# Optimization experiments

Measured on AMD Instinct MI355X. Metric: run time of the kernel, lower is better.

## Reference

```python
import jax, jax.numpy as jnp
import numpy as np

NEG_SLOPE = 0.2
CLAMP = 1e9

C, N, T, IN_F = 8, 1024, 3, 64
H, OUT_F = 4, 64
E = 65536


def setup_inputs() -> dict:
    key = jax.random.key(0)
    k1, k2, k3, k4, k5 = jax.random.split(key, 5)
    edge_idx = jax.random.randint(k1, (2, E), 0, C * N, dtype=jnp.int64)
    node_feats = jax.random.normal(k2, (C, N, T, IN_F), dtype=jnp.float32)
    # xavier-ish scaling for parameters
    fc = jax.random.normal(k3, (T, IN_F, OUT_F * H), dtype=jnp.float32) * (2.0 / (IN_F + OUT_F * H)) ** 0.5
    attn_src = jax.random.normal(k4, (1, H, OUT_F * T), dtype=jnp.float32) * 0.1
    attn_dst = jax.random.normal(k5, (1, H, OUT_F * T), dtype=jnp.float32) * 0.1
    return {"edge_idx": edge_idx, "node_feats": node_feats, "fc": fc,
            "attn_src": attn_src, "attn_dst": attn_dst}


def reference(edge_idx, node_feats, fc, attn_src, attn_dst):
    c, n, t, f_in = node_feats.shape
    h = attn_src.shape[1]
    f_out = fc.shape[2] // h
    cn = c * n

    # per-node-type linear transform: (cn, t, in) x (t, in, h*out) -> (cn, t, h*out)
    hs = node_feats.reshape(cn, t, f_in)
    feat = jnp.einsum('bji,jik->bjk', hs, fc)

    # replicate the torch permute/reshape sequence exactly (row-major reshapes)
    x = feat.reshape(c, n, t, f_out * h)
    x = jnp.transpose(x, (0, 2, 1, 3))                  # (c, t, n, h*out)
    x = x.reshape(c, n, t, h, f_out)                    # torch .reshape on permuted copy
    x = jnp.transpose(x, (0, 1, 3, 2, 4))               # (c, n, h, t, out)
    feat_flat = x.reshape(cn, h, t * f_out)             # feat_src = feat_dst

    # node masks from edge endpoints (scatter 1s on rows)
    msrc = jnp.zeros((cn,), node_feats.dtype).at[edge_idx[0]].set(1.0)
    mdst = jnp.zeros((cn,), node_feats.dtype).at[edge_idx[1]].set(1.0)
    feat_src = feat_flat * msrc[:, None, None]
    feat_dst = feat_flat * mdst[:, None, None]

    a_src = jnp.clip(feat_src * attn_src, -CLAMP, CLAMP).reshape(c, n, h, f_out * t).sum(-1)
    a_dst = jnp.clip(feat_dst * attn_dst, -CLAMP, CLAMP).reshape(c, n, h, f_out * t).sum(-1)

    a = a_src[:, :, None, :] + a_dst[:, None, :, :]     # (c, n, n, h)
    a = jnp.where(a >= 0, a, NEG_SLOPE * a)             # leaky relu
    a = jnp.clip(a, -CLAMP, CLAMP)
    a = jax.nn.softmax(a, axis=0)                       # softmax over conformers (dim=0, as in source)

    fd = feat_dst.reshape(c, n, h, t * f_out)
    m = jnp.einsum('cvuh,cuhf->cvhf', a, fd)            # (c, n, h, t*out)
    m = jax.nn.relu(m)
    outs = m.reshape(c, n, h, t, f_out).sum(axis=2)     # (c, n, t, out)
    return outs, a
```

## Files before the change

### kernel.cpp

```cpp
#include <hip/hip_runtime.h>
#include <stdint.h>

#define CC 8
#define NN 1024
#define CN 8192
#define NE 65536
#define NEG_SLOPE 0.2f

typedef __attribute__((ext_vector_type(8))) short bf16x8;
typedef __attribute__((ext_vector_type(4))) float f32x4;

__device__ __forceinline__ ushort f2bfu(float x) {
    unsigned u = __float_as_uint(x);
    unsigned r = u + 0x7fffu + ((u >> 16) & 1u);
    return (ushort)(r >> 16);
}

__global__ void k_scatter(const int* __restrict__ edges,
                          float* __restrict__ msrc, float* __restrict__ mdst) {
    int e = blockIdx.x * 256 + threadIdx.x;
    if (e < NE) {
        msrc[edges[e]] = 1.0f;
        mdst[edges[NE + e]] = 1.0f;
    }
}

__global__ void __launch_bounds__(256) k_feat(const float* __restrict__ nf,
                                              const float* __restrict__ fc,
                                              float* __restrict__ feat) {
    __shared__ float sFC[64][132];
    __shared__ float sHT[64][36];
    int t = threadIdx.x;
    int tt = blockIdx.y;
    int kh = blockIdx.x & 1;
    int r0 = (blockIdx.x >> 1) * 32;
    {
        const float* fcp = fc + tt * 16384 + kh * 128;
        #pragma unroll
        for (int i = 0; i < 8; ++i) {
            int f4 = t + 256 * i;
            int row = f4 >> 5, c4 = f4 & 31;
            *(float4*)&sFC[row][c4 * 4] = *(const float4*)(fcp + row * 256 + c4 * 4);
        }
    }
    {
        #pragma unroll
        for (int i = 0; i < 2; ++i) {
            int f4 = t + 256 * i;
            int r = f4 >> 4, c4 = f4 & 15;
            float4 v = *(const float4*)(nf + (size_t)(r0 + r) * 192 + tt * 64 + c4 * 4);
            sHT[c4 * 4 + 0][r] = v.x;
            sHT[c4 * 4 + 1][r] = v.y;
            sHT[c4 * 4 + 2][r] = v.z;
            sHT[c4 * 4 + 3][r] = v.w;
        }
    }
    __syncthreads();
    int rg = t >> 5;
    int kg = t & 31;
    float acc[4][4];
    #pragma unroll
    for (int a = 0; a < 4; ++a)
        #pragma unroll
        for (int b = 0; b < 4; ++b) acc[a][b] = 0.f;
    #pragma unroll 4
    for (int i = 0; i < 64; ++i) {
        float4 hv = *(const float4*)&sHT[i][rg * 4];
        float4 fv = *(const float4*)&sFC[i][kg * 4];
        const float* fp = (const float*)&fv;
        #pragma unroll
        for (int b = 0; b < 4; ++b) {
            acc[0][b] += hv.x * fp[b];
            acc[1][b] += hv.y * fp[b];
            acc[2][b] += hv.z * fp[b];
            acc[3][b] += hv.w * fp[b];
        }
    }
    #pragma unroll
    for (int a = 0; a < 4; ++a) {
        int b = r0 + rg * 4 + a;
        int c = b >> 10, n = b & 1023;
        float4 vv = {acc[a][0], acc[a][1], acc[a][2], acc[a][3]};
        *(float4*)(feat + (size_t)c * 786432 + (size_t)tt * 262144 + n * 256 + kh * 128 + kg * 4) = vv;
    }
}

__global__ void __launch_bounds__(256) k_remap(const float* __restrict__ feat,
                        const float* __restrict__ attn_src, const float* __restrict__ attn_dst,
                        const float* __restrict__ msrc, const float* __restrict__ mdst,
                        ushort* __restrict__ fd, float* __restrict__ a_src, float* __restrict__ a_dst) {
    int b = blockIdx.x;
    int c = b >> 10, n2 = b & 1023;
    int t = threadIdx.x;
    int h = t >> 6, f = t & 63;
    float md = mdst[b], ms = msrc[b];
    const float* fp = feat + (size_t)c * 786432 + (size_t)n2 * 768;
    float ssum = 0.f, dsum = 0.f;
    #pragma unroll
    for (int t2 = 0; t2 < 3; ++t2) {
        float val = fp[t2 * 256 + t];
        int j = t2 * 64 + f;
        ssum += val * attn_src[h * 192 + j];
        dsum += val * attn_dst[h * 192 + j];
        fd[((size_t)(c * 4 + h) * 1024 + n2) * 192 + j] = f2bfu(val * md);
    }
    #pragma unroll
    for (int o = 32; o > 0; o >>= 1) {
        ssum += __shfl_down(ssum, o, 64);
        dsum += __shfl_down(dsum, o, 64);
    }
    if (f == 0) {
        a_src[(b << 2) + h] = ssum * ms;
        a_dst[(b << 2) + h] = dsum * md;
    }
}

__global__ void k_trans(const ushort* __restrict__ fd, ushort* __restrict__ fdt) {
    __shared__ ushort tile[64][68];
    int ch = blockIdx.z;
    int u0 = blockIdx.x * 64, j0 = blockIdx.y * 64;
    int t = threadIdx.x;
    const ushort* src = fd + (size_t)ch * (1024 * 192) + (size_t)u0 * 192 + j0;
    #pragma unroll
    for (int i = 0; i < 2; ++i) {
        int vid = t + 256 * i;
        int r = vid >> 3, ccol = (vid & 7) * 8;
        uint4 v = *(const uint4*)(src + (size_t)r * 192 + ccol);
        const ushort* us = (const ushort*)&v;
        #pragma unroll
        for (int jj = 0; jj < 8; ++jj) tile[r][ccol + jj] = us[jj];
    }
    __syncthreads();
    ushort* dst = fdt + (size_t)ch * (192 * 1024) + (size_t)j0 * 1024 + u0;
    #pragma unroll
    for (int i = 0; i < 2; ++i) {
        int vid = t + 256 * i;
        int jr = vid >> 3, uc = (vid & 7) * 8;
        ushort tmp[8];
        #pragma unroll
        for (int jj = 0; jj < 8; ++jj) tmp[jj] = tile[uc + jj][jr];
        *(uint4*)(dst + (size_t)jr * 1024 + uc) = *(const uint4*)tmp;
    }
}

__global__ void __launch_bounds__(256) k_att(const float* __restrict__ a_src,
                                             const float* __restrict__ a_dst,
                                             float* __restrict__ a_out, ushort* __restrict__ Abuf) {
    __shared__ float sAS[32];
    int v = blockIdx.x;
    int t = threadIdx.x;
    if (t < 32) sAS[t] = a_src[((t >> 2) * 1024 + v) * 4 + (t & 3)];
    __syncthreads();
    int u0 = blockIdx.y * 512 + t * 2;

    float mx0[4], mx1[4];
    #pragma unroll
    for (int h = 0; h < 4; ++h) { mx0[h] = -1e30f; mx1[h] = -1e30f; }
    #pragma unroll
    for (int c = 0; c < 8; ++c) {
        float4 d0 = *(const float4*)(a_dst + ((c << 10) + u0) * 4);
        float4 d1 = *(const float4*)(a_dst + ((c << 10) + u0 + 1) * 4);
        const float* dp0 = (const float*)&d0;
        const float* dp1 = (const float*)&d1;
        #pragma unroll
        for (int h = 0; h < 4; ++h) {
            float as = sAS[c * 4 + h];
            mx0[h] = fmaxf(mx0[h], as + dp0[h]);
            mx1[h] = fmaxf(mx1[h], as + dp1[h]);
        }
    }
    #pragma unroll
    for (int h = 0; h < 4; ++h) {
        float x = mx0[h];
        x = (x >= 0.f) ? x : NEG_SLOPE * x;
        mx0[h] = fminf(fmaxf(x, -1e9f), 1e9f);
        float y = mx1[h];
        y = (y >= 0.f) ? y : NEG_SLOPE * y;
        mx1[h] = fminf(fmaxf(y, -1e9f), 1e9f);
    }

    float s0[4] = {0.f, 0.f, 0.f, 0.f}, s1[4] = {0.f, 0.f, 0.f, 0.f};
    #pragma unroll
    for (int c = 0; c < 8; ++c) {
        float4 d0 = *(const float4*)(a_dst + ((c << 10) + u0) * 4);
        float4 d1 = *(const float4*)(a_dst + ((c << 10) + u0 + 1) * 4);
        const float* dp0 = (const float*)&d0;
        const float* dp1 = (const float*)&d1;
        #pragma unroll
        for (int h = 0; h < 4; ++h) {
            float as = sAS[c * 4 + h];
            float x = as + dp0[h];
            x = (x >= 0.f) ? x : NEG_SLOPE * x;
            x = fminf(fmaxf(x, -1e9f), 1e9f);
            s0[h] += __expf(x - mx0[h]);
            float y = as + dp1[h];
            y = (y >= 0.f) ? y : NEG_SLOPE * y;
            y = fminf(fmaxf(y, -1e9f), 1e9f);
            s1[h] += __expf(y - mx1[h]);
        }
    }
    float r0[4], r1[4];
    #pragma unroll
    for (int h = 0; h < 4; ++h) { r0[h] = 1.f / s0[h]; r1[h] = 1.f / s1[h]; }

    #pragma unroll
    for (int c = 0; c < 8; ++c) {
        float4 d0 = *(const float4*)(a_dst + ((c << 10) + u0) * 4);
        float4 d1 = *(const float4*)(a_dst + ((c << 10) + u0 + 1) * 4);
        const float* dp0 = (const float*)&d0;
        const float* dp1 = (const float*)&d1;
        float w0[4], w1[4];
        unsigned packs[4];
        #pragma unroll
        for (int h = 0; h < 4; ++h) {
            float as = sAS[c * 4 + h];
            float x = as + dp0[h];
            x = (x >= 0.f) ? x : NEG_SLOPE * x;
            x = fminf(fmaxf(x, -1e9f), 1e9f);
            float p0 = __expf(x - mx0[h]) * r0[h];
            float y = as + dp1[h];
            y = (y >= 0.f) ? y : NEG_SLOPE * y;
            y = fminf(fmaxf(y, -1e9f), 1e9f);
            float p1 = __expf(y - mx1[h]) * r1[h];
            w0[h] = p0; w1[h] = p1;
            packs[h] = (unsigned)f2bfu(p0) | ((unsigned)f2bfu(p1) << 16);
        }
        float* ao = a_out + ((size_t)((c << 10) + v) * 1024 + u0) * 4;
        *(float4*)ao = *(const float4*)w0;
        *((float4*)ao + 1) = *(const float4*)w1;
        #pragma unroll
        for (int h = 0; h < 4; ++h)
            *(unsigned*)(Abuf + (size_t)((c * 4 + h) * 1024 + v) * 1024 + u0) = packs[h];
    }
}

__global__ void __launch_bounds__(256) k_gemm(const ushort* __restrict__ A,
                                              const ushort* __restrict__ B,
                                              float* __restrict__ Mout) {
    __shared__ ushort sA[64 * 72];
    __shared__ ushort sB[192 * 72];
    int ch = blockIdx.y;
    int v0 = blockIdx.x * 64;
    int t = threadIdx.x;
    const ushort* pA = A + (size_t)ch * (1024 * 1024) + (size_t)v0 * 1024;
    const ushort* pB = B + (size_t)ch * (192 * 1024);
    int wid = t >> 6, lane = t & 63;
    int wn = wid * 48;
    int lm = lane & 15, lq = lane >> 4;
    f32x4 acc[4][3];
    #pragma unroll
    for (int i = 0; i < 4; ++i)
        #pragma unroll
        for (int j = 0; j < 3; ++j)
            acc[i][j] = (f32x4){0.f, 0.f, 0.f, 0.f};
    for (int kk = 0; kk < 1024; kk += 64) {
        #pragma unroll
        for (int i = 0; i < 2; ++i) {
            int cid = t + 256 * i;
            int r = cid >> 3, kc = cid & 7;
            uint4 vv = *(const uint4*)(pA + (size_t)r * 1024 + kk + kc * 8);
            *(uint4*)&sA[r * 72 + kc * 8] = vv;
        }
        #pragma unroll
        for (int i = 0; i < 6; ++i) {
            int cid = t + 256 * i;
            int r = cid >> 3, kc = cid & 7;
            uint4 vv = *(const uint4*)(pB + (size_t)r * 1024 + kk + kc * 8);
            *(uint4*)&sB[r * 72 + kc * 8] = vv;
        }
        __syncthreads();
        #pragma unroll
        for (int ks = 0; ks < 64; ks += 32) {
            bf16x8 af[4], bg[3];
            #pragma unroll
            for (int i = 0; i < 4; ++i)
                af[i] = *(const bf16x8*)&sA[(i * 16 + lm) * 72 + ks + lq * 8];
            #pragma unroll
            for (int j = 0; j < 3; ++j)
                bg[j] = *(const bf16x8*)&sB[(wn + j * 16 + lm) * 72 + ks + lq * 8];
            #pragma unroll
            for (int i = 0; i < 4; ++i)
                #pragma unroll
                for (int j = 0; j < 3; ++j)
                    acc[i][j] = __builtin_amdgcn_mfma_f32_16x16x32_bf16(af[i], bg[j], acc[i][j], 0, 0, 0);
        }
        __syncthreads();
    }
    float* pM = Mout + (size_t)ch * 196608 + (size_t)v0 * 192;
    #pragma unroll
    for (int i = 0; i < 4; ++i)
        #pragma unroll
        for (int r = 0; r < 4; ++r) {
            int row = i * 16 + lq * 4 + r;
            #pragma unroll
            for (int j = 0; j < 3; ++j)
                pM[(size_t)row * 192 + wn + j * 16 + lm] = acc[i][j][r];
        }
}

__global__ void k_out(const float* __restrict__ Mm, float* __restrict__ outp) {
    int b = blockIdx.x;
    int c = b >> 10, v = b & 1023;
    int tf = threadIdx.x;
    float s = 0.f;
    #pragma unroll
    for (int h = 0; h < 4; ++h) {
        float x = Mm[(size_t)(c * 4 + h) * 196608 + (size_t)v * 192 + tf];
        s += fmaxf(x, 0.f);
    }
    outp[(size_t)b * 192 + tf] = s;
}

extern "C" void kernel_launch(void* const* d_in, const int* in_sizes, int n_in,
                              void* d_out, int out_size, void* d_ws, size_t ws_size,
                              hipStream_t stream) {
    const int*   edges  = (const int*)d_in[0];
    const float* nf     = (const float*)d_in[1];
    const float* fc     = (const float*)d_in[2];
    const float* asrc_w = (const float*)d_in[3];
    const float* adst_w = (const float*)d_in[4];
    float* outp  = (float*)d_out;
    float* a_out = outp + 1572864;

    char* ws = (char*)d_ws;
    float*  msrc  = (float*)(ws + 0);
    float*  mdst  = (float*)(ws + 32768);
    float*  a_src = (float*)(ws + 65536);
    float*  a_dst = (float*)(ws + 196608);
    ushort* fdt   = (ushort*)(ws + 327680);
    float*  feat  = (float*)(ws + 12910592);
    float*  Mm    = feat;
    ushort* Abuf  = (ushort*)(ws + 38076416);
    ushort* fd    = Abuf;

    hipMemsetAsync(msrc, 0, 65536, stream);
    k_scatter<<<dim3(256), dim3(256), 0, stream>>>(edges, msrc, mdst);
    k_feat<<<dim3(512, 3), dim3(256), 0, stream>>>(nf, fc, feat);
    k_remap<<<dim3(8192), dim3(256), 0, stream>>>(feat, asrc_w, adst_w, msrc, mdst, fd, a_src, a_dst);
    k_trans<<<dim3(16, 3, 32), dim3(256), 0, stream>>>(fd, fdt);
    k_att<<<dim3(1024, 2), dim3(256), 0, stream>>>(a_src, a_dst, a_out, Abuf);
    k_gemm<<<dim3(16, 32), dim3(256), 0, stream>>>(Abuf, fdt, Mm);
    k_out<<<dim3(8192), dim3(192), 0, stream>>>(Mm, outp);
}
```

Measured before the change: 282.8 us.

## Fuse remap and transpose into one kernel via shared-memory staging

Merges the remap kernel (attention logits plus bf16 masked feature write) and the separate transpose kernel into a single kernel. Each block stages a 64-node by 256-column tile in LDS and writes the transposed fdt layout directly. This removes the intermediate fd buffer round trip and one launch. Partial logits per time slice are combined with atomicAdd, so the memset now also zeroes a_src/a_dst, and the summation order changes.

```diff
diff --git a/kernel.cpp b/kernel.cpp
--- a/kernel.cpp
+++ b/kernel.cpp
@@ -85,62 +85,43 @@
     }
 }
 
-__global__ void __launch_bounds__(256) k_remap(const float* __restrict__ feat,
+__global__ void __launch_bounds__(256) k_rt(const float* __restrict__ feat,
                         const float* __restrict__ attn_src, const float* __restrict__ attn_dst,
                         const float* __restrict__ msrc, const float* __restrict__ mdst,
-                        ushort* __restrict__ fd, float* __restrict__ a_src, float* __restrict__ a_dst) {
-    int b = blockIdx.x;
-    int c = b >> 10, n2 = b & 1023;
+                        ushort* __restrict__ fdt, float* __restrict__ a_src, float* __restrict__ a_dst) {
+    __shared__ ushort T[22560];
+    int u0 = blockIdx.x * 64;
+    int t2 = blockIdx.y;
+    int c  = blockIdx.z;
     int t = threadIdx.x;
-    int h = t >> 6, f = t & 63;
+    int nl = t >> 2, q = t & 3;
+    int b = (c << 10) + u0 + nl;
     float md = mdst[b], ms = msrc[b];
-    const float* fp = feat + (size_t)c * 786432 + (size_t)n2 * 768;
+    const float* fp  = feat + (size_t)c * 786432 + (size_t)(u0 + nl) * 768 + t2 * 256 + q * 64;
+    const float* wsp = attn_src + q * 192 + t2 * 64;
+    const float* wdp = attn_dst + q * 192 + t2 * 64;
     float ssum = 0.f, dsum = 0.f;
     #pragma unroll
-    for (int t2 = 0; t2 < 3; ++t2) {
-        float val = fp[t2 * 256 + t];
-        int j = t2 * 64 + f;
-        ssum += val * attn_src[h * 192 + j];
-        dsum += val * attn_dst[h * 192 + j];
-        fd[((size_t)(c * 4 + h) * 1024 + n2) * 192 + j] = f2bfu(val * md);
-    }
-    #pragma unroll
-    for (int o = 32; o > 0; o >>= 1) {
-        ssum += __shfl_down(ssum, o, 64);
-        dsum += __shfl_down(dsum, o, 64);
-    }
-    if (f == 0) {
-        a_src[(b << 2) + h] = ssum * ms;
-        a_dst[(b << 2) + h] = dsum * md;
-    }
-}
-
-__global__ void k_trans(const ushort* __restrict__ fd, ushort* __restrict__ fdt) {
-    __shared__ ushort tile[64][68];
-    int ch = blockIdx.z;
-    int u0 = blockIdx.x * 64, j0 = blockIdx.y * 64;
-    int t = threadIdx.x;
-    const ushort* src = fd + (size_t)ch * (1024 * 192) + (size_t)u0 * 192 + j0;
-    #pragma unroll
-    for (int i = 0; i < 2; ++i) {
-        int vid = t + 256 * i;
-        int r = vid >> 3, ccol = (vid & 7) * 8;
-        uint4 v = *(const uint4*)(src + (size_t)r * 192 + ccol);
-        const ushort* us = (const ushort*)&v;
-        #pragma unroll
-        for (int jj = 0; jj < 8; ++jj) tile[r][ccol + jj] = us[jj];
-    }
+    for (int i4 = 0; i4 < 16; ++i4) {
+        float4 v = *(const float4*)(fp + i4 * 4);
+        const float* vv = (const float*)&v;
+        #pragma unroll
+        for (int k = 0; k < 4; ++k) {
+            int f = i4 * 4 + k;
+            ssum += vv[k] * wsp[f];
+            dsum += vv[k] * wdp[f];
+            T[(q * 64 + f) * 88 + q * 16 + nl] = f2bfu(vv[k] * md);
+        }
+    }
+    atomicAdd(&a_src[(b << 2) + q], ssum * ms);
+    atomicAdd(&a_dst[(b << 2) + q], dsum * md);
     __syncthreads();
-    ushort* dst = fdt + (size_t)ch * (192 * 1024) + (size_t)j0 * 1024 + u0;
-    #pragma unroll
-    for (int i = 0; i < 2; ++i) {
-        int vid = t + 256 * i;
-        int jr = vid >> 3, uc = (vid & 7) * 8;
-        ushort tmp[8];
-        #pragma unroll
-        for (int jj = 0; jj < 8; ++jj) tmp[jj] = tile[uc + jj][jr];
-        *(uint4*)(dst + (size_t)jr * 1024 + uc) = *(const uint4*)tmp;
-    }
+    int h2 = t >> 6, j = t & 63;
+    const ushort* row = &T[(h2 * 64 + j) * 88 + h2 * 16];
+    ushort* dst = fdt + (size_t)((c * 4 + h2) * 192 + t2 * 64 + j) * 1024 + u0;
+    #pragma unroll
+    for (int i = 0; i < 8; ++i)
+        *(uint4*)(dst + i * 8) = *(const uint4*)(row + i * 8);
 }
 
 __global__ void __launch_bounds__(256) k_att(const float* __restrict__ a_src,
@@ -331,13 +312,11 @@
     float*  feat  = (float*)(ws + 12910592);
     float*  Mm    = feat;
     ushort* Abuf  = (ushort*)(ws + 38076416);
-    ushort* fd    = Abuf;
-
-    hipMemsetAsync(msrc, 0, 65536, stream);
+
+    hipMemsetAsync(msrc, 0, 327680, stream);
     k_scatter<<<dim3(256), dim3(256), 0, stream>>>(edges, msrc, mdst);
     k_feat<<<dim3(512, 3), dim3(256), 0, stream>>>(nf, fc, feat);
-    k_remap<<<dim3(8192), dim3(256), 0, stream>>>(feat, asrc_w, adst_w, msrc, mdst, fd, a_src, a_dst);
-    k_trans<<<dim3(16, 3, 32), dim3(256), 0, stream>>>(fd, fdt);
+    k_rt<<<dim3(16, 3, 8), dim3(256), 0, stream>>>(feat, asrc_w, adst_w, msrc, mdst, fdt, a_src, a_dst);
     k_att<<<dim3(1024, 2), dim3(256), 0, stream>>>(a_src, a_dst, a_out, Abuf);
     k_gemm<<<dim3(16, 32), dim3(256), 0, stream>>>(Abuf, fdt, Mm);
     k_out<<<dim3(8192), dim3(192), 0, stream>>>(Mm, outp);
```

Result: no change. 287.9 us (+1.8%).
